# Optimization experiments

Measured on AMD Instinct MI355X. Metric: run time of the kernel, lower is better.

Reference implementation:

```python
import jax, jax.numpy as jnp
import numpy as np
import math

DIM_PER_HEAD = 64

def setup_inputs() -> dict:
    key = jax.random.key(0)
    k1, k2, k3, k4 = jax.random.split(key, 4)
    B, H, S, D = 2, 16, 2048, 64
    mat1 = jax.random.normal(k1, (B, H, S, D), dtype=jnp.float32)
    mat2 = jax.random.normal(k2, (B, H, S, D), dtype=jnp.float32)
    mat3 = jax.random.normal(k3, (B, H, S, D), dtype=jnp.float32)
    bias = jax.random.normal(k4, (1, 1, S, S), dtype=jnp.float32)
    return {"mat1": mat1, "mat2": mat2, "mat3": mat3, "bias": bias}

def reference(mat1, mat2, mat3, bias) -> jnp.ndarray:
    # scale Q, scores = QK^T + bias, softmax over last dim, then @ V
    scale = 1.0 / math.sqrt(DIM_PER_HEAD)
    qk = jnp.einsum('bhqd,bhkd->bhqk', mat1 * scale, mat2)  # [B,H,S,S]
    scores = jax.nn.softmax(qk + bias, axis=-1)
    return jnp.einsum('bhqk,bhkd->bhqd', scores, mat3)
```

## Files before the change

kernel.cpp:

```cpp
#include <hip/hip_runtime.h>
#include <hip/hip_bf16.h>


#define SEQ 2048
#define DH  64
#define BHN 32
#define LOG2E 1.44269504088896f

typedef __attribute__((ext_vector_type(8))) short bf16x8;
typedef __attribute__((ext_vector_type(4))) float f32x4;
typedef __attribute__((ext_vector_type(8))) short short8v;

__device__ inline short f2b(float x) {
    union { float f; unsigned u; } v; v.f = x;
    unsigned r = v.u + 0x7fff + ((v.u >> 16) & 1);
    return (short)(r >> 16);
}

__device__ inline void gl_lds16(const void* g, void* l) {
    __builtin_amdgcn_global_load_lds(
        (const __attribute__((address_space(1))) void*)g,
        (__attribute__((address_space(3))) void*)l, 16, 0, 0);
}

__device__ __host__ inline int phi(int r) {
    return 32 * (r >> 5) + 16 * ((r >> 2) & 1) + 4 * ((r >> 3) & 3) + (r & 3);
}

__global__ __launch_bounds__(256)
void prep_kv(const float* __restrict__ K, const float* __restrict__ V,
             short* __restrict__ Kb, short* __restrict__ Vt) {
    __shared__ short t[64 * 72];
    const int tid = threadIdx.x;
    const int bh = blockIdx.x >> 5, st = blockIdx.x & 31, s0 = st * 64;

    {
        const float* Kp = K + ((size_t)bh * SEQ + s0) * DH;
        short* Ko = Kb + ((size_t)bh * SEQ + s0) * DH;
        #pragma unroll
        for (int i = 0; i < 2; ++i) {
            size_t o = (size_t)(tid + i * 256) * 8;
            f32x4 a = *(const f32x4*)(Kp + o);
            f32x4 b = *(const f32x4*)(Kp + o + 4);
            short8v s;
            #pragma unroll
            for (int j = 0; j < 4; ++j) { s[j] = f2b(a[j]); s[4 + j] = f2b(b[j]); }
            *(short8v*)(Ko + o) = s;
        }
    }

    const float* Vb = V + (size_t)bh * SEQ * DH + (size_t)s0 * DH;
    #pragma unroll
    for (int i = 0; i < 4; ++i) {
        int c = tid + i * 256, s = c >> 4, c4 = c & 15;
        f32x4 v = *(const f32x4*)(Vb + s * DH + c4 * 4);
        #pragma unroll
        for (int j = 0; j < 4; ++j) t[s * 72 + c4 * 4 + j] = f2b(v[j]);
    }
    __syncthreads();
    const int d = tid >> 2, part = tid & 3;
    short* outp = Vt + (size_t)bh * DH * SEQ + (size_t)d * SEQ + s0 + part * 16;
    #pragma unroll
    for (int h = 0; h < 2; ++h) {
        short8v w;
        #pragma unroll
        for (int u = 0; u < 8; ++u) {
            int rho = part * 16 + h * 8 + u;
            w[u] = t[phi(rho) * 72 + d];
        }
        *(short8v*)(outp + h * 8) = w;
    }
}

__global__ __launch_bounds__(256, 4)
void mha_main(const float* __restrict__ Q, const float* __restrict__ Bias,
              const short* __restrict__ Kb, const short* __restrict__ Vt,
              float* __restrict__ Out)
{
    __shared__ short ka[64 * DH];
    __shared__ short kbuf[64 * DH];
    __shared__ short va[64 * DH];
    __shared__ short vbuf[64 * DH];

    const int tid = threadIdx.x, lane = tid & 63, wave = tid >> 6;
    const int l15 = lane & 15, l4 = lane >> 4;
    const int qb = blockIdx.x & 31, bh = blockIdx.x >> 5;
    const int q0 = qb * 64;

    const float* Qb = Q + (size_t)bh * SEQ * DH;
    const short* Kh = Kb + (size_t)bh * SEQ * DH;
    const short* Vh = Vt + (size_t)bh * DH * SEQ;
    float* Ob = Out + (size_t)bh * SEQ * DH;

    bf16x8 qf[2];
    {
        const float* qp = Qb + (size_t)(q0 + wave * 16 + l15) * DH;
        #pragma unroll
        for (int ks = 0; ks < 2; ++ks) {
            short tmp[8];
            #pragma unroll
            for (int j = 0; j < 8; ++j) tmp[j] = f2b(qp[ks * 32 + l4 * 8 + j] * (0.125f * LOG2E));
            qf[ks] = *reinterpret_cast<bf16x8*>(tmp);
        }
    }

    f32x4 o_acc[4];
    #pragma unroll
    for (int dt = 0; dt < 4; ++dt) o_acc[dt] = f32x4{0.f, 0.f, 0.f, 0.f};
    float l_part = 0.f;

    const short *kg0, *kg1, *vg0, *vg1;
    int off0, off1;
    {
        int s0_ = wave * 64 + lane, r0 = s0_ >> 3, c0 = s0_ & 7, g0 = c0 ^ (r0 & 7);
        int s1_ = 256 + wave * 64 + lane, r1 = s1_ >> 3, c1 = s1_ & 7, g1 = c1 ^ (r1 & 7);
        kg0 = Kh + (size_t)r0 * DH + g0 * 8;
        vg0 = Vh + (size_t)r0 * SEQ + g0 * 8;
        kg1 = Kh + (size_t)r1 * DH + g1 * 8;
        vg1 = Vh + (size_t)r1 * SEQ + g1 * 8;
        off0 = (wave * 64) * 8;
        off1 = (256 + wave * 64) * 8;
    }
    const float* bp0 = Bias + (size_t)(q0 + wave * 16 + l15) * SEQ + l4 * 4;
    const int swz = l15 & 7;

    gl_lds16(kg0, ka + off0);
    gl_lds16(kg1, ka + off1);
    gl_lds16(vg0, va + off0);
    gl_lds16(vg1, va + off1);

    auto tile = [&](int kt, const short* kc, const short* vc,
                    short* knx, short* vnx) {
        f32x4 bv[4];
        const float* bp = bp0 + kt * 64;
        #pragma unroll
        for (int nt = 0; nt < 4; ++nt)
            bv[nt] = *(const f32x4*)(bp + nt * 16);

        const int kn = (kt + 1) & 31;
        gl_lds16(kg0 + (size_t)kn * 64 * DH, knx + off0);
        gl_lds16(kg1 + (size_t)kn * 64 * DH, knx + off1);
        gl_lds16(vg0 + kn * 64, vnx + off0);
        gl_lds16(vg1 + kn * 64, vnx + off1);

        asm volatile("s_waitcnt vmcnt(8)\n\ts_barrier" ::: "memory");

        f32x4 sacc[4];
        #pragma unroll
        for (int nt = 0; nt < 4; ++nt) sacc[nt] = f32x4{0.f, 0.f, 0.f, 0.f};
        #pragma unroll
        for (int ks = 0; ks < 2; ++ks)
            #pragma unroll
            for (int nt = 0; nt < 4; ++nt) {
                int cc = (ks * 4 + l4) ^ swz;
                bf16x8 kf = *(const bf16x8*)&kc[(nt * 16 + l15) * DH + cc * 8];
                sacc[nt] = __builtin_amdgcn_mfma_f32_16x16x32_bf16(kf, qf[ks], sacc[nt], 0, 0, 0);
            }

        unsigned pk[4][2];
        #pragma unroll
        for (int nt = 0; nt < 4; ++nt) {
            float pv[4];
            #pragma unroll
            for (int r = 0; r < 4; ++r) {
                pv[r] = __builtin_amdgcn_exp2f(__builtin_fmaf(bv[nt][r], LOG2E, sacc[nt][r]));
                l_part += pv[r];
            }
            #pragma unroll
            for (int rp = 0; rp < 2; ++rp) {
                __hip_bfloat162 h2 = __float22bfloat162_rn(float2{pv[2 * rp], pv[2 * rp + 1]});
                pk[nt][rp] = *reinterpret_cast<unsigned*>(&h2);
            }
        }

        #pragma unroll
        for (int ks = 0; ks < 2; ++ks) {
            union { bf16x8 v; unsigned u[4]; } af;
            af.u[0] = pk[2 * ks][0]; af.u[1] = pk[2 * ks][1];
            af.u[2] = pk[2 * ks + 1][0]; af.u[3] = pk[2 * ks + 1][1];
            #pragma unroll
            for (int dt = 0; dt < 4; ++dt) {
                int cc = (ks * 4 + l4) ^ swz;
                bf16x8 vf = *(const bf16x8*)&vc[(dt * 16 + l15) * DH + cc * 8];
                o_acc[dt] = __builtin_amdgcn_mfma_f32_16x16x32_bf16(af.v, vf, o_acc[dt], 0, 0, 0);
            }
        }

        asm volatile("s_barrier" ::: "memory");
    };

    for (int kt = 0; kt < SEQ / 64; kt += 2) {
        tile(kt,     ka,   va,   kbuf, vbuf);
        tile(kt + 1, kbuf, vbuf, ka,   va);
    }

    l_part += __shfl_xor(l_part, 16, 64);
    l_part += __shfl_xor(l_part, 32, 64);

    #pragma unroll
    for (int r = 0; r < 4; ++r) {
        float lr = __shfl(l_part, l4 * 4 + r, 64);
        float inv = 1.0f / lr;
        float* op = Ob + (size_t)(q0 + wave * 16 + l4 * 4 + r) * DH + l15;
        #pragma unroll
        for (int dt = 0; dt < 4; ++dt) op[dt * 16] = o_acc[dt][r] * inv;
    }
}

extern "C" void kernel_launch(void* const* d_in, const int* in_sizes, int n_in,
                              void* d_out, int out_size, void* d_ws, size_t ws_size,
                              hipStream_t stream) {
    const float* Q    = (const float*)d_in[0];
    const float* K    = (const float*)d_in[1];
    const float* V    = (const float*)d_in[2];
    const float* Bias = (const float*)d_in[3];
    float* O          = (float*)d_out;

    short* Kb = (short*)d_ws;
    short* Vt = Kb + (size_t)BHN * SEQ * DH;

    prep_kv<<<dim3(BHN * 32), dim3(256), 0, stream>>>(K, V, Kb, Vt);
    mha_main<<<dim3(BHN * 32), dim3(256), 0, stream>>>(Q, Bias, Kb, Vt, O);
}
```

Baseline: 184.1 us.

## Preload K/V fragments to registers, prefetch bias a tile ahead, single barrier

Each tile iteration now starts with one __syncthreads. All K and V MFMA fragments for the current tile are then read from LDS into registers before the async global-to-LDS loads for the next tile are issued. This removes the second per-tile barrier and the hand-written partial vmcnt wait. Bias values for the next tile are loaded right after the softmax exponentials, so their global latency is hidden behind the PV MFMAs. The cost is about 64 extra live VGPRs for the fragments under a 4-blocks-per-CU launch bound, which risks spills or lower occupancy, and the barrier now waits for all outstanding memory operations.

```diff
diff --git a/kernel.cpp b/kernel.cpp
--- a/kernel.cpp
+++ b/kernel.cpp
@@ -77,10 +77,10 @@
               const short* __restrict__ Kb, const short* __restrict__ Vt,
               float* __restrict__ Out)
 {
-    __shared__ short ka[64 * DH];
-    __shared__ short kbuf[64 * DH];
-    __shared__ short va[64 * DH];
-    __shared__ short vbuf[64 * DH];
+    __shared__ short kA[64 * DH];
+    __shared__ short kB[64 * DH];
+    __shared__ short vA[64 * DH];
+    __shared__ short vB[64 * DH];
 
     const int tid = threadIdx.x, lane = tid & 63, wave = tid >> 6;
     const int l15 = lane & 15, l4 = lane >> 4;
@@ -124,18 +124,35 @@
     const float* bp0 = Bias + (size_t)(q0 + wave * 16 + l15) * SEQ + l4 * 4;
     const int swz = l15 & 7;
 
-    gl_lds16(kg0, ka + off0);
-    gl_lds16(kg1, ka + off1);
-    gl_lds16(vg0, va + off0);
-    gl_lds16(vg1, va + off1);
-
-    auto tile = [&](int kt, const short* kc, const short* vc,
+    gl_lds16(kg0, kA + off0);
+    gl_lds16(kg1, kA + off1);
+    gl_lds16(vg0, vA + off0);
+    gl_lds16(vg1, vA + off1);
+    f32x4 bv[4];
+    #pragma unroll
+    for (int nt = 0; nt < 4; ++nt)
+        bv[nt] = *(const f32x4*)(bp0 + nt * 16);
+
+    auto body = [&](int kt, const short* kc, const short* vc,
                     short* knx, short* vnx) {
-        f32x4 bv[4];
-        const float* bp = bp0 + kt * 64;
-        #pragma unroll
-        for (int nt = 0; nt < 4; ++nt)
-            bv[nt] = *(const f32x4*)(bp + nt * 16);
+        __syncthreads();
+
+        bf16x8 kfr[2][4];
+        #pragma unroll
+        for (int ks = 0; ks < 2; ++ks)
+            #pragma unroll
+            for (int nt = 0; nt < 4; ++nt) {
+                int cc = (ks * 4 + l4) ^ swz;
+                kfr[ks][nt] = *(const bf16x8*)&kc[(nt * 16 + l15) * DH + cc * 8];
+            }
+        bf16x8 vfr[2][4];
+        #pragma unroll
+        for (int ks = 0; ks < 2; ++ks)
+            #pragma unroll
+            for (int dt = 0; dt < 4; ++dt) {
+                int cc = (ks * 4 + l4) ^ swz;
+                vfr[ks][dt] = *(const bf16x8*)&vc[(dt * 16 + l15) * DH + cc * 8];
+            }
 
         const int kn = (kt + 1) & 31;
         gl_lds16(kg0 + (size_t)kn * 64 * DH, knx + off0);
@@ -143,19 +160,14 @@
         gl_lds16(vg0 + kn * 64, vnx + off0);
         gl_lds16(vg1 + kn * 64, vnx + off1);
 
-        asm volatile("s_waitcnt vmcnt(8)\n\ts_barrier" ::: "memory");
-
         f32x4 sacc[4];
         #pragma unroll
         for (int nt = 0; nt < 4; ++nt) sacc[nt] = f32x4{0.f, 0.f, 0.f, 0.f};
         #pragma unroll
         for (int ks = 0; ks < 2; ++ks)
             #pragma unroll
-            for (int nt = 0; nt < 4; ++nt) {
-                int cc = (ks * 4 + l4) ^ swz;
-                bf16x8 kf = *(const bf16x8*)&kc[(nt * 16 + l15) * DH + cc * 8];
-                sacc[nt] = __builtin_amdgcn_mfma_f32_16x16x32_bf16(kf, qf[ks], sacc[nt], 0, 0, 0);
-            }
+            for (int nt = 0; nt < 4; ++nt)
+                sacc[nt] = __builtin_amdgcn_mfma_f32_16x16x32_bf16(kfr[ks][nt], qf[ks], sacc[nt], 0, 0, 0);
 
         unsigned pk[4][2];
         #pragma unroll
@@ -171,6 +183,13 @@
                 __hip_bfloat162 h2 = __float22bfloat162_rn(float2{pv[2 * rp], pv[2 * rp + 1]});
                 pk[nt][rp] = *reinterpret_cast<unsigned*>(&h2);
             }
+        }
+
+        {
+            const float* bp = bp0 + kn * 64;
+            #pragma unroll
+            for (int nt = 0; nt < 4; ++nt)
+                bv[nt] = *(const f32x4*)(bp + nt * 16);
         }
 
         #pragma unroll
@@ -179,19 +198,14 @@
             af.u[0] = pk[2 * ks][0]; af.u[1] = pk[2 * ks][1];
             af.u[2] = pk[2 * ks + 1][0]; af.u[3] = pk[2 * ks + 1][1];
             #pragma unroll
-            for (int dt = 0; dt < 4; ++dt) {
-                int cc = (ks * 4 + l4) ^ swz;
-                bf16x8 vf = *(const bf16x8*)&vc[(dt * 16 + l15) * DH + cc * 8];
-                o_acc[dt] = __builtin_amdgcn_mfma_f32_16x16x32_bf16(af.v, vf, o_acc[dt], 0, 0, 0);
-            }
-        }
-
-        asm volatile("s_barrier" ::: "memory");
+            for (int dt = 0; dt < 4; ++dt)
+                o_acc[dt] = __builtin_amdgcn_mfma_f32_16x16x32_bf16(af.v, vfr[ks][dt], o_acc[dt], 0, 0, 0);
+        }
     };
 
     for (int kt = 0; kt < SEQ / 64; kt += 2) {
-        tile(kt,     ka,   va,   kbuf, vbuf);
-        tile(kt + 1, kbuf, vbuf, ka,   va);
+        body(kt,     kA, vA, kB, vB);
+        body(kt + 1, kB, vB, kA, vA);
     }
 
     l_part += __shfl_xor(l_part, 16, 64);
```

After: 184.0 us. Within noise of the previous version (-0.1%).
